# Kernel optimization log

Hardware: AMD Instinct MI355X
Metric: run time of the kernel (lower is better)

The kernel has to match this reference:

```python
import jax, jax.numpy as jnp
import numpy as np

N = 100000      # nodes
F_IN = 256      # num_node_features
E = 1600000     # edges (before self-loops)
DIMS = [F_IN, 128, 100, 32, 2]  # GCNConv layer widths


def _glorot(key, fan_in, fan_out):
    s = jnp.sqrt(6.0 / (fan_in + fan_out))
    return jax.random.uniform(key, (fan_in, fan_out), jnp.float32, -s, s)


def setup_inputs() -> dict:
    key = jax.random.key(0)
    ks = jax.random.split(key, 10)
    x = jax.random.normal(ks[0], (N, F_IN), jnp.float32)
    edge_index = jax.random.randint(ks[1], (2, E), 0, N, jnp.int32)
    inp = {"x": x, "edge_index": edge_index}
    for i in range(4):
        inp[f"W{i+1}"] = _glorot(ks[2 + 2 * i], DIMS[i], DIMS[i + 1])
        inp[f"b{i+1}"] = jnp.zeros((DIMS[i + 1],), jnp.float32)
    return inp


def reference(x, edge_index, W1, b1, W2, b2, W3, b3, W4, b4):
    n = x.shape[0]
    loops = jnp.arange(n, dtype=edge_index.dtype)
    src = jnp.concatenate([edge_index[0], loops])  # [E+N]
    dst = jnp.concatenate([edge_index[1], loops])
    # symmetric normalization: deg^-1/2[src] * deg^-1/2[dst] (self-loops included)
    deg = jax.ops.segment_sum(jnp.ones_like(src, x.dtype), dst, num_segments=n)
    dis = jax.lax.rsqrt(jnp.maximum(deg, 1.0))
    norm = (dis[src] * dis[dst])[:, None]  # [E+N, 1]

    def conv(h, W, b):
        h = h @ W                                      # [N, out]
        msg = h[src] * norm                            # gather + scale [E+N, out]
        return jax.ops.segment_sum(msg, dst, num_segments=n) + b

    h = jax.nn.leaky_relu(conv(x, W1, b1), negative_slope=0.1)
    h = jax.nn.leaky_relu(conv(h, W2, b2), negative_slope=0.1)
    h = jax.nn.leaky_relu(conv(h, W3, b3), negative_slope=0.1)
    h = conv(h, W4, b4)
    return jax.nn.softmax(h, axis=-1)
```

## Files before the change

kernel.cpp:

```cpp
#include <hip/hip_runtime.h>
#include <math.h>


typedef unsigned short ushort_t;
typedef unsigned int   uint_t;
typedef short  bf16x8 __attribute__((ext_vector_type(8)));
typedef float  f32x4  __attribute__((ext_vector_type(4)));

#define BKT_SHIFT 8
#define BKT_CAP   5120
#define BIN_CHUNK 4096

__device__ __forceinline__ ushort_t f2bf(float f) {
    union { float f; uint_t u; } v; v.f = f;
    uint_t u = v.u;
    u += 0x7fffu + ((u >> 16) & 1u);
    return (ushort_t)(u >> 16);
}
__device__ __forceinline__ float bflo(uint_t u) {
    union { uint_t q; float f; } v; v.q = u << 16; return v.f;
}
__device__ __forceinline__ float bfhi(uint_t u) {
    union { uint_t q; float f; } v; v.q = u & 0xffff0000u; return v.f;
}


__global__ __launch_bounds__(256) void bin_kernel(const int* __restrict__ srcArr,
                                                  const int* __restrict__ dstArr,
                                                  int* __restrict__ bkt_cursor,
                                                  uint_t* __restrict__ staging,
                                                  int E, int nb) {
    __shared__ int hist[512];
    __shared__ int base[512];
    for (int b = threadIdx.x; b < 512; b += 256) hist[b] = 0;
    __syncthreads();
    const int e0 = blockIdx.x * BIN_CHUNK;
    int sv[16], dv[16];
    #pragma unroll
    for (int k = 0; k < 16; ++k) {
        int e = e0 + k * 256 + threadIdx.x;
        if (e < E) {
            sv[k] = srcArr[e];
            dv[k] = dstArr[e];
            atomicAdd(&hist[dv[k] >> BKT_SHIFT], 1);
        } else {
            sv[k] = 0; dv[k] = -1;
        }
    }
    __syncthreads();
    for (int b = threadIdx.x; b < nb; b += 256) {
        int h = hist[b];
        base[b] = h ? atomicAdd(&bkt_cursor[b], h) : 0;
    }
    __syncthreads();
    for (int b = threadIdx.x; b < 512; b += 256) hist[b] = 0;
    __syncthreads();
    #pragma unroll
    for (int k = 0; k < 16; ++k) {
        if (dv[k] >= 0) {
            int b = dv[k] >> BKT_SHIFT;
            int p = atomicAdd(&hist[b], 1);
            int idx = base[b] + p;
            if (idx < BKT_CAP)
                staging[(size_t)b * BKT_CAP + idx] =
                    ((uint_t)sv[k] << 8) | (uint_t)(dv[k] & 255);
        }
    }
}

__global__ __launch_bounds__(512) void bucket_scan_kernel(const int* __restrict__ bkt_cursor,
                                                          int* __restrict__ bkt_base,
                                                          int* __restrict__ row_start,
                                                          int nbkt, int n) {
    __shared__ int buf[512];
    int v = ((int)threadIdx.x < nbkt) ? min(bkt_cursor[threadIdx.x], BKT_CAP) : 0;
    buf[threadIdx.x] = v;
    __syncthreads();
    for (int off = 1; off < 512; off <<= 1) {
        int t = (threadIdx.x >= (unsigned)off) ? buf[threadIdx.x - off] : 0;
        __syncthreads();
        buf[threadIdx.x] += t;
        __syncthreads();
    }
    if ((int)threadIdx.x < nbkt) bkt_base[threadIdx.x] = buf[threadIdx.x] - v;
    if ((int)threadIdx.x == nbkt - 1) row_start[n] = buf[threadIdx.x];
}

__global__ __launch_bounds__(256) void csr_build2_kernel(const uint_t* __restrict__ staging,
                                                         const int* __restrict__ bkt_cursor,
                                                         const int* __restrict__ bkt_base,
                                                         int* __restrict__ row_start,
                                                         float* __restrict__ dis,
                                                         int* __restrict__ csr_src, int n) {
    __shared__ int cnt[256];
    __shared__ int buf[256];
    __shared__ int rsS[256];
    __shared__ int seg[BKT_CAP];
    const int t  = threadIdx.x;
    const int b  = blockIdx.x;
    const int lo = b << BKT_SHIFT;
    const int nl = min(256, n - lo);
    cnt[t] = 0;
    __syncthreads();
    const int cntE = min(bkt_cursor[b], BKT_CAP);
    for (int e = t; e < cntE; e += 256) {
        uint_t p = staging[(size_t)b * BKT_CAP + e];
        atomicAdd(&cnt[p & 255u], 1);
    }
    __syncthreads();
    const int v = cnt[t];
    buf[t] = v;
    __syncthreads();
    for (int off = 1; off < 256; off <<= 1) {
        int tt = (t >= off) ? buf[t - off] : 0;
        __syncthreads();
        buf[t] += tt;
        __syncthreads();
    }
    rsS[t] = buf[t] - v;
    const int sbase = bkt_base[b];
    if (t < nl) {
        row_start[lo + t] = sbase + (buf[t] - v);
        dis[lo + t] = rsqrtf((float)(v + 1));
    }
    cnt[t] = 0;
    __syncthreads();
    for (int e = t; e < cntE; e += 256) {
        uint_t p = staging[(size_t)b * BKT_CAP + e];
        int ln = (int)(p & 255u);
        int q  = atomicAdd(&cnt[ln], 1);
        seg[rsS[ln] + q] = (int)(p >> 8);
    }
    __syncthreads();
    for (int i = t; i < cntE; i += 256) csr_src[sbase + i] = seg[i];
}

__global__ void wt_all_kernel(const float* __restrict__ W1, const float* __restrict__ W2,
                              const float* __restrict__ W3,
                              ushort_t* __restrict__ Wt1, ushort_t* __restrict__ Wt2,
                              ushort_t* __restrict__ Wt3) {
    int idx = blockIdx.x * blockDim.x + threadIdx.x;
    if (idx < 32768) {
        int nn = idx >> 8, k = idx & 255;
        Wt1[idx] = f2bf(W1[(size_t)k * 128 + nn]);
    } else if (idx < 49152) {
        int j = idx - 32768;
        int nn = j >> 7, k = j & 127;
        float v = (nn < 100) ? W2[(size_t)k * 100 + nn] : 0.f;
        Wt2[j] = f2bf(v);
    } else if (idx < 57344) {
        int j = idx - 49152;
        int nn = j >> 7, k = j & 127;
        float v = (k < 100 && nn < 32) ? W3[(size_t)k * 32 + nn] : 0.f;
        Wt3[j] = f2bf(v);
    }
}

template <bool A_FP32, int NFR>
__global__ __launch_bounds__(256) void gemm_tile(const void* __restrict__ Av,
                                                 const ushort_t* __restrict__ Bt,
                                                 ushort_t* __restrict__ C,
                                                 const float* __restrict__ dis,
                                                 int M, int K, int lda, int ldb, int ldc) {
    constexpr int BN = NFR * 32;
    __shared__ __attribute__((aligned(16))) ushort_t As[64][72];
    __shared__ __attribute__((aligned(16))) ushort_t Bs[BN][72];

    const int t    = threadIdx.x;
    const int lane = t & 63;
    const int w    = t >> 6;
    const int wm   = w >> 1, wn = w & 1;
    const int m0   = blockIdx.x * 64;
    const int rsel = lane & 15;
    const int q    = lane >> 4;

    f32x4 acc[2][NFR];
    #pragma unroll
    for (int mi = 0; mi < 2; ++mi)
        #pragma unroll
        for (int ni = 0; ni < NFR; ++ni) acc[mi][ni] = (f32x4){0.f, 0.f, 0.f, 0.f};

    const int srow = t >> 3;
    const int scol = (t & 7) * 8;

    for (int k0 = 0; k0 < K; k0 += 64) {
        #pragma unroll
        for (int it = 0; it < 2; ++it) {
            int r = srow + it * 32;
            int gm = m0 + r;
            bf16x8 v = {0, 0, 0, 0, 0, 0, 0, 0};
            if (gm < M) {
                if (A_FP32) {
                    const float* A = (const float*)Av;
                    const float4 f0 = *(const float4*)(A + (size_t)gm * lda + k0 + scol);
                    const float4 f1 = *(const float4*)(A + (size_t)gm * lda + k0 + scol + 4);
                    ushort_t o[8] = { f2bf(f0.x), f2bf(f0.y), f2bf(f0.z), f2bf(f0.w),
                                      f2bf(f1.x), f2bf(f1.y), f2bf(f1.z), f2bf(f1.w) };
                    v = *(const bf16x8*)o;
                } else {
                    const ushort_t* A = (const ushort_t*)Av;
                    v = *(const bf16x8*)(A + (size_t)gm * lda + k0 + scol);
                }
            }
            *(bf16x8*)&As[r][scol] = v;
        }
        #pragma unroll
        for (int it = 0; it < BN / 32; ++it) {
            int r = srow + it * 32;
            bf16x8 v = *(const bf16x8*)(Bt + (size_t)r * ldb + k0 + scol);
            *(bf16x8*)&Bs[r][scol] = v;
        }
        __syncthreads();
        #pragma unroll
        for (int ks = 0; ks < 2; ++ks) {
            const int kc = ks * 32 + q * 8;
            bf16x8 af[2], bfr[NFR];
            #pragma unroll
            for (int mi = 0; mi < 2; ++mi)
                af[mi] = *(const bf16x8*)&As[wm * 32 + mi * 16 + rsel][kc];
            #pragma unroll
            for (int ni = 0; ni < NFR; ++ni)
                bfr[ni] = *(const bf16x8*)&Bs[wn * (BN / 2) + ni * 16 + rsel][kc];
            #pragma unroll
            for (int mi = 0; mi < 2; ++mi)
                #pragma unroll
                for (int ni = 0; ni < NFR; ++ni)
                    acc[mi][ni] = __builtin_amdgcn_mfma_f32_16x16x32_bf16(
                        bfr[ni], af[mi], acc[mi][ni], 0, 0, 0);
        }
        __syncthreads();
    }

    #pragma unroll
    for (int mi = 0; mi < 2; ++mi) {
        const int gm = m0 + wm * 32 + mi * 16 + rsel;
        if (gm >= M) continue;
        const float d = dis[gm];
        #pragma unroll
        for (int ni = 0; ni < NFR; ++ni) {
            uint2 o;
            o.x = (uint_t)f2bf(acc[mi][ni][0] * d) | ((uint_t)f2bf(acc[mi][ni][1] * d) << 16);
            o.y = (uint_t)f2bf(acc[mi][ni][2] * d) | ((uint_t)f2bf(acc[mi][ni][3] * d) << 16);
            *(uint2*)(C + (size_t)gm * ldc + wn * (BN / 2) + ni * 16 + q * 4) = o;
        }
    }
}

template <int F>
__global__ void aggregate128_kernel(const ushort_t* __restrict__ h, const int* __restrict__ row_start,
                                    const int* __restrict__ csr_src,
                                    const float* __restrict__ dis, const float* __restrict__ bias,
                                    ushort_t* __restrict__ out, int n) {
    const int lane = threadIdx.x & 63;
    const int grp  = lane >> 4;
    const int node = blockIdx.x * 16 + (int)(threadIdx.x >> 6) * 4 + grp;
    if (node >= n) return;
    const uint_t fbb = (uint_t)(lane & 15) << 4;
    const char* hb = (const char*)h;
    float a[8];
    #pragma unroll
    for (int j = 0; j < 8; ++j) a[j] = 0.f;

    int i = row_start[node];
    const int end = row_start[node + 1];

#define LOADR(S) (*(const uint4*)(hb + (((uint_t)(S) << 8) + fbb)))
#define ACC8(U)                                                     \
    do {                                                            \
        a[0] += bflo((U).x); a[1] += bfhi((U).x);                   \
        a[2] += bflo((U).y); a[3] += bfhi((U).y);                   \
        a[4] += bflo((U).z); a[5] += bfhi((U).z);                   \
        a[6] += bflo((U).w); a[7] += bfhi((U).w);                   \
    } while (0)

    for (; i + 8 <= end; i += 8) {
        int s0 = csr_src[i];
        int s1 = csr_src[i + 1];
        int s2 = csr_src[i + 2];
        int s3 = csr_src[i + 3];
        int s4 = csr_src[i + 4];
        int s5 = csr_src[i + 5];
        int s6 = csr_src[i + 6];
        int s7 = csr_src[i + 7];
        uint4 u0 = LOADR(s0);
        uint4 u1 = LOADR(s1);
        uint4 u2 = LOADR(s2);
        uint4 u3 = LOADR(s3);
        uint4 u4 = LOADR(s4);
        uint4 u5 = LOADR(s5);
        uint4 u6 = LOADR(s6);
        uint4 u7 = LOADR(s7);
        ACC8(u0); ACC8(u1); ACC8(u2); ACC8(u3);
        ACC8(u4); ACC8(u5); ACC8(u6); ACC8(u7);
    }
    for (; i + 4 <= end; i += 4) {
        int s0 = csr_src[i];
        int s1 = csr_src[i + 1];
        int s2 = csr_src[i + 2];
        int s3 = csr_src[i + 3];
        uint4 u0 = LOADR(s0);
        uint4 u1 = LOADR(s1);
        uint4 u2 = LOADR(s2);
        uint4 u3 = LOADR(s3);
        ACC8(u0); ACC8(u1); ACC8(u2); ACC8(u3);
    }
    for (; i < end; ++i) {
        uint4 u = LOADR(csr_src[i]);
        ACC8(u);
    }
    {
        uint4 su = LOADR(node);
        ACC8(su);
    }
    float dn = dis[node];
    const int fb = (lane & 15) * 8;
    #pragma unroll
    for (int j = 0; j < 8; ++j) {
        float b = (fb + j < F) ? bias[fb + j] : 0.f;
        float v = a[j] * dn + b;
        v = (v > 0.f) ? v : 0.1f * v;
        if (fb + j >= F) v = 0.f;
        a[j] = v;
    }
    uint4 o;
    o.x = (uint_t)f2bf(a[0]) | ((uint_t)f2bf(a[1]) << 16);
    o.y = (uint_t)f2bf(a[2]) | ((uint_t)f2bf(a[3]) << 16);
    o.z = (uint_t)f2bf(a[4]) | ((uint_t)f2bf(a[5]) << 16);
    o.w = (uint_t)f2bf(a[6]) | ((uint_t)f2bf(a[7]) << 16);
    *(uint4*)((char*)out + (((uint_t)node << 8) + fbb)) = o;
#undef ACC8
#undef LOADR
}

__global__ void aggregate32_kernel(const ushort_t* __restrict__ h, const int* __restrict__ row_start,
                                   const int* __restrict__ csr_src,
                                   const float* __restrict__ dis, const float* __restrict__ bias,
                                   ushort_t* __restrict__ out, int n) {
    int lane16 = threadIdx.x & 15;
    int node = blockIdx.x * (blockDim.x >> 4) + (threadIdx.x >> 4);
    if (node >= n) return;
    const uint_t fbb = (uint_t)lane16 << 2;
    const char* hb = (const char*)h;
#define LOADR32(S) (*(const uint_t*)(hb + (((uint_t)(S) << 6) + fbb)))
    uint_t v = LOADR32(node);
    float acc0 = bflo(v);
    float acc1 = bfhi(v);
    int i = row_start[node], end = row_start[node + 1];
    for (; i + 4 <= end; i += 4) {
        uint_t u0 = LOADR32(csr_src[i]);
        uint_t u1 = LOADR32(csr_src[i + 1]);
        uint_t u2 = LOADR32(csr_src[i + 2]);
        uint_t u3 = LOADR32(csr_src[i + 3]);
        acc0 += bflo(u0) + bflo(u1) + bflo(u2) + bflo(u3);
        acc1 += bfhi(u0) + bfhi(u1) + bfhi(u2) + bfhi(u3);
    }
    for (; i < end; ++i) {
        uint_t u = LOADR32(csr_src[i]);
        acc0 += bflo(u); acc1 += bfhi(u);
    }
#undef LOADR32
    float dn = dis[node];
    const int f0 = 2 * lane16;
    acc0 = acc0 * dn + bias[f0];
    acc1 = acc1 * dn + bias[f0 + 1];
    acc0 = (acc0 > 0.f) ? acc0 : 0.1f * acc0;
    acc1 = (acc1 > 0.f) ? acc1 : 0.1f * acc1;
    uint_t o = (uint_t)f2bf(acc0) | ((uint_t)f2bf(acc1) << 16);
    *(uint_t*)((char*)out + (((uint_t)node << 6) + fbb)) = o;
}

__global__ void gemm32x2_kernel(const ushort_t* __restrict__ H, const float* __restrict__ W4,
                                const float* __restrict__ dis, float* __restrict__ C, int n) {
    int node = blockIdx.x * blockDim.x + threadIdx.x;
    if (node >= n) return;
    const uint_t* row = (const uint_t*)(H + (size_t)node * 32);
    float a0 = 0.f, a1 = 0.f;
    #pragma unroll
    for (int k2 = 0; k2 < 16; ++k2) {
        uint_t u = row[k2];
        float x0 = bflo(u), x1 = bfhi(u);
        int k = 2 * k2;
        a0 += x0 * W4[k * 2]     + x1 * W4[(k + 1) * 2];
        a1 += x0 * W4[k * 2 + 1] + x1 * W4[(k + 1) * 2 + 1];
    }
    float d = dis[node];
    C[2 * (size_t)node]     = a0 * d;
    C[2 * (size_t)node + 1] = a1 * d;
}

__global__ void aggregate2_softmax_kernel(const float* __restrict__ h, const int* __restrict__ row_start,
                                          const int* __restrict__ csr_src,
                                          const float* __restrict__ dis, const float* __restrict__ bias,
                                          float* __restrict__ out, int n) {
    int node = blockIdx.x * blockDim.x + threadIdx.x;
    if (node >= n) return;
    const char* hb = (const char*)h;
    float a0 = h[2 * (size_t)node];
    float a1 = h[2 * (size_t)node + 1];
    int beg = row_start[node], end = row_start[node + 1];
    for (int i = beg; i < end; ++i) {
        uint_t off = (uint_t)csr_src[i] << 3;
        float2 u = *(const float2*)(hb + off);
        a0 += u.x;
        a1 += u.y;
    }
    float dn = dis[node];
    a0 = a0 * dn + bias[0];
    a1 = a1 * dn + bias[1];
    float m  = fmaxf(a0, a1);
    float e0 = expf(a0 - m), e1 = expf(a1 - m);
    float inv = 1.f / (e0 + e1);
    out[2 * (size_t)node]     = e0 * inv;
    out[2 * (size_t)node + 1] = e1 * inv;
}


extern "C" void kernel_launch(void* const* d_in, const int* in_sizes, int n_in,
                              void* d_out, int out_size, void* d_ws, size_t ws_size,
                              hipStream_t stream) {
    const float* x  = (const float*)d_in[0];
    const int*   ei = (const int*)d_in[1];
    const float* W1 = (const float*)d_in[2];
    const float* b1 = (const float*)d_in[3];
    const float* W2 = (const float*)d_in[4];
    const float* b2 = (const float*)d_in[5];
    const float* W3 = (const float*)d_in[6];
    const float* b3 = (const float*)d_in[7];
    const float* W4 = (const float*)d_in[8];
    const float* b4 = (const float*)d_in[9];

    const int N = in_sizes[0] / 256;
    const int E = in_sizes[1] / 2;
    const int* srcA = ei;
    const int* dstA = ei + E;
    const int nbkt = (N + 255) >> BKT_SHIFT;

    char* ws = (char*)d_ws;
    size_t off = 0;
    auto alloc = [&](size_t bytes) {
        void* p = ws + off;
        off = (off + bytes + 255) & ~(size_t)255;
        return p;
    };
    float*    dis        = (float*)alloc((size_t)N * 4);
    int*      row_start  = (int*)alloc((size_t)(N + 1) * 4);
    int*      bkt_cursor = (int*)alloc(512 * 4);
    int*      bkt_base   = (int*)alloc(512 * 4);
    int*      csr_src    = (int*)alloc((size_t)E * 4);
    uint_t*   staging    = (uint_t*)alloc((size_t)nbkt * BKT_CAP * 4);
    ushort_t* bufA       = (ushort_t*)alloc((size_t)N * 128 * 2);
    ushort_t* bufB       = (ushort_t*)alloc((size_t)N * 128 * 2);
    float*    C4         = (float*)alloc((size_t)N * 2 * 4);
    ushort_t* Wt1        = (ushort_t*)alloc((size_t)128 * 256 * 2);
    ushort_t* Wt2        = (ushort_t*)alloc((size_t)128 * 128 * 2);
    ushort_t* Wt3        = (ushort_t*)alloc((size_t)64 * 128 * 2);
    (void)ws_size;

    hipMemsetAsync(bkt_cursor, 0, 512 * 4, stream);

    bin_kernel<<<(E + BIN_CHUNK - 1) / BIN_CHUNK, 256, 0, stream>>>(
        srcA, dstA, bkt_cursor, staging, E, nbkt);
    bucket_scan_kernel<<<1, 512, 0, stream>>>(bkt_cursor, bkt_base, row_start, nbkt, N);
    csr_build2_kernel<<<nbkt, 256, 0, stream>>>(staging, bkt_cursor, bkt_base,
                                                row_start, dis, csr_src, N);

    wt_all_kernel<<<(57344 + 255) / 256, 256, 0, stream>>>(W1, W2, W3, Wt1, Wt2, Wt3);

    const int gx = (N + 63) / 64;
    const int aggBlocks128 = (N + 15) / 16;
    const int aggBlocks32  = (N + 15) / 16;

    gemm_tile<true, 4><<<gx, 256, 0, stream>>>(x, Wt1, bufA, dis, N, 256, 256, 256, 128);
    aggregate128_kernel<128><<<aggBlocks128, 256, 0, stream>>>(
        bufA, row_start, csr_src, dis, b1, bufB, N);
    gemm_tile<false, 4><<<gx, 256, 0, stream>>>(bufB, Wt2, bufA, dis, N, 128, 128, 128, 128);
    aggregate128_kernel<100><<<aggBlocks128, 256, 0, stream>>>(
        bufA, row_start, csr_src, dis, b2, bufB, N);
    gemm_tile<false, 1><<<gx, 256, 0, stream>>>(bufB, Wt3, bufA, dis, N, 128, 128, 128, 32);
    aggregate32_kernel<<<aggBlocks32, 256, 0, stream>>>(
        bufA, row_start, csr_src, dis, b3, bufB, N);
    gemm32x2_kernel<<<(N + 255) / 256, 256, 0, stream>>>(bufB, W4, dis, C4, N);
    aggregate2_softmax_kernel<<<(N + 255) / 256, 256, 0, stream>>>(
        C4, row_start, csr_src, dis, b4, (float*)d_out, N);
}
```

Measured before the change: 279.2 us.

## Shrink layer-2 row stride to 112 and fuse W4 projection into aggregate32

```diff
diff --git a/kernel.cpp b/kernel.cpp
--- a/kernel.cpp
+++ b/kernel.cpp
@@ -238,15 +238,17 @@
         const float d = dis[gm];
         #pragma unroll
         for (int ni = 0; ni < NFR; ++ni) {
+            const int cb = wn * (BN / 2) + ni * 16 + q * 4;
+            if (cb >= ldc) continue;
             uint2 o;
             o.x = (uint_t)f2bf(acc[mi][ni][0] * d) | ((uint_t)f2bf(acc[mi][ni][1] * d) << 16);
             o.y = (uint_t)f2bf(acc[mi][ni][2] * d) | ((uint_t)f2bf(acc[mi][ni][3] * d) << 16);
-            *(uint2*)(C + (size_t)gm * ldc + wn * (BN / 2) + ni * 16 + q * 4) = o;
-        }
-    }
-}
-
-template <int F>
+            *(uint2*)(C + (size_t)gm * ldc + cb) = o;
+        }
+    }
+}
+
+template <int F, int CHUNKS>
 __global__ void aggregate128_kernel(const ushort_t* __restrict__ h, const int* __restrict__ row_start,
                                     const int* __restrict__ csr_src,
                                     const float* __restrict__ dis, const float* __restrict__ bias,
@@ -255,7 +257,10 @@
     const int grp  = lane >> 4;
     const int node = blockIdx.x * 16 + (int)(threadIdx.x >> 6) * 4 + grp;
     if (node >= n) return;
-    const uint_t fbb = (uint_t)(lane & 15) << 4;
+    const int l16 = lane & 15;
+    if (l16 >= CHUNKS) return;
+    const uint_t STRIDE = (uint_t)CHUNKS * 16u;
+    const uint_t fbb = (uint_t)l16 << 4;
     const char* hb = (const char*)h;
     float a[8];
     #pragma unroll
@@ -264,7 +269,7 @@
     int i = row_start[node];
     const int end = row_start[node + 1];
 
-#define LOADR(S) (*(const uint4*)(hb + (((uint_t)(S) << 8) + fbb)))
+#define LOADR(S) (*(const uint4*)(hb + ((uint_t)(S) * STRIDE + fbb)))
 #define ACC8(U)                                                     \
     do {                                                            \
         a[0] += bflo((U).x); a[1] += bfhi((U).x);                   \
@@ -313,7 +318,7 @@
         ACC8(su);
     }
     float dn = dis[node];
-    const int fb = (lane & 15) * 8;
+    const int fb = l16 * 8;
     #pragma unroll
     for (int j = 0; j < 8; ++j) {
         float b = (fb + j < F) ? bias[fb + j] : 0.f;
@@ -327,15 +332,15 @@
     o.y = (uint_t)f2bf(a[2]) | ((uint_t)f2bf(a[3]) << 16);
     o.z = (uint_t)f2bf(a[4]) | ((uint_t)f2bf(a[5]) << 16);
     o.w = (uint_t)f2bf(a[6]) | ((uint_t)f2bf(a[7]) << 16);
-    *(uint4*)((char*)out + (((uint_t)node << 8) + fbb)) = o;
+    *(uint4*)((char*)out + ((uint_t)node * STRIDE + fbb)) = o;
 #undef ACC8
 #undef LOADR
 }
 
-__global__ void aggregate32_kernel(const ushort_t* __restrict__ h, const int* __restrict__ row_start,
-                                   const int* __restrict__ csr_src,
-                                   const float* __restrict__ dis, const float* __restrict__ bias,
-                                   ushort_t* __restrict__ out, int n) {
+__global__ void aggregate32_w4_kernel(const ushort_t* __restrict__ h, const int* __restrict__ row_start,
+                                      const int* __restrict__ csr_src,
+                                      const float* __restrict__ dis, const float* __restrict__ bias,
+                                      const float* __restrict__ W4, float* __restrict__ C4, int n) {
     int lane16 = threadIdx.x & 15;
     int node = blockIdx.x * (blockDim.x >> 4) + (threadIdx.x >> 4);
     if (node >= n) return;
@@ -365,27 +370,18 @@
     acc1 = acc1 * dn + bias[f0 + 1];
     acc0 = (acc0 > 0.f) ? acc0 : 0.1f * acc0;
     acc1 = (acc1 > 0.f) ? acc1 : 0.1f * acc1;
-    uint_t o = (uint_t)f2bf(acc0) | ((uint_t)f2bf(acc1) << 16);
-    *(uint_t*)((char*)out + (((uint_t)node << 6) + fbb)) = o;
-}
-
-__global__ void gemm32x2_kernel(const ushort_t* __restrict__ H, const float* __restrict__ W4,
-                                const float* __restrict__ dis, float* __restrict__ C, int n) {
-    int node = blockIdx.x * blockDim.x + threadIdx.x;
-    if (node >= n) return;
-    const uint_t* row = (const uint_t*)(H + (size_t)node * 32);
-    float a0 = 0.f, a1 = 0.f;
-    #pragma unroll
-    for (int k2 = 0; k2 < 16; ++k2) {
-        uint_t u = row[k2];
-        float x0 = bflo(u), x1 = bfhi(u);
-        int k = 2 * k2;
-        a0 += x0 * W4[k * 2]     + x1 * W4[(k + 1) * 2];
-        a1 += x0 * W4[k * 2 + 1] + x1 * W4[(k + 1) * 2 + 1];
-    }
-    float d = dis[node];
-    C[2 * (size_t)node]     = a0 * d;
-    C[2 * (size_t)node + 1] = a1 * d;
+    const float4 w = *(const float4*)(W4 + 4 * lane16);
+    float p0 = acc0 * w.x + acc1 * w.z;
+    float p1 = acc0 * w.y + acc1 * w.w;
+    #pragma unroll
+    for (int m = 1; m < 16; m <<= 1) {
+        p0 += __shfl_xor(p0, m);
+        p1 += __shfl_xor(p1, m);
+    }
+    if (lane16 == 0) {
+        float2 o = { p0 * dn, p1 * dn };
+        *(float2*)(C4 + 2 * (size_t)node) = o;
+    }
 }
 
 __global__ void aggregate2_softmax_kernel(const float* __restrict__ h, const int* __restrict__ row_start,
@@ -467,19 +463,17 @@
     wt_all_kernel<<<(57344 + 255) / 256, 256, 0, stream>>>(W1, W2, W3, Wt1, Wt2, Wt3);
 
     const int gx = (N + 63) / 64;
-    const int aggBlocks128 = (N + 15) / 16;
-    const int aggBlocks32  = (N + 15) / 16;
+    const int aggBlocks = (N + 15) / 16;
 
     gemm_tile<true, 4><<<gx, 256, 0, stream>>>(x, Wt1, bufA, dis, N, 256, 256, 256, 128);
-    aggregate128_kernel<128><<<aggBlocks128, 256, 0, stream>>>(
+    aggregate128_kernel<128, 16><<<aggBlocks, 256, 0, stream>>>(
         bufA, row_start, csr_src, dis, b1, bufB, N);
-    gemm_tile<false, 4><<<gx, 256, 0, stream>>>(bufB, Wt2, bufA, dis, N, 128, 128, 128, 128);
-    aggregate128_kernel<100><<<aggBlocks128, 256, 0, stream>>>(
+    gemm_tile<false, 4><<<gx, 256, 0, stream>>>(bufB, Wt2, bufA, dis, N, 128, 128, 128, 112);
+    aggregate128_kernel<100, 14><<<aggBlocks, 256, 0, stream>>>(
         bufA, row_start, csr_src, dis, b2, bufB, N);
-    gemm_tile<false, 1><<<gx, 256, 0, stream>>>(bufB, Wt3, bufA, dis, N, 128, 128, 128, 32);
-    aggregate32_kernel<<<aggBlocks32, 256, 0, stream>>>(
-        bufA, row_start, csr_src, dis, b3, bufB, N);
-    gemm32x2_kernel<<<(N + 255) / 256, 256, 0, stream>>>(bufB, W4, dis, C4, N);
+    gemm_tile<false, 1><<<gx, 256, 0, stream>>>(bufB, Wt3, bufA, dis, N, 128, 112, 128, 32);
+    aggregate32_w4_kernel<<<aggBlocks, 256, 0, stream>>>(
+        bufA, row_start, csr_src, dis, b3, W4, C4, N);
     aggregate2_softmax_kernel<<<(N + 255) / 256, 256, 0, stream>>>(
         C4, row_start, csr_src, dis, b4, (float*)d_out, N);
 }
```

New measurement: 279.0 us. Within noise of the previous version (-0.1%).
